# Performance work log

Hardware: AMD Instinct MI355X
Metric: run time of the kernel (lower is better)

## Reference

```python
import jax, jax.numpy as jnp
import numpy as np

B, S, D, H = 4, 2048, 1024, 16
DK = D // H
THETA = 10000.0


def apply_rope(x, pos, theta):
    # x: [B, H, S, DK], pos: [S] int
    d = x.shape[-1]
    inv_freq = theta ** (-jnp.arange(0, d, 2, dtype=jnp.float32) / d)  # [d/2]
    ang = pos.astype(jnp.float32)[:, None] * inv_freq[None, :]          # [S, d/2]
    cos, sin = jnp.cos(ang), jnp.sin(ang)
    x1 = x[..., 0::2]
    x2 = x[..., 1::2]
    r1 = x1 * cos - x2 * sin
    r2 = x1 * sin + x2 * cos
    return jnp.stack([r1, r2], axis=-1).reshape(x.shape)


def setup_inputs() -> dict:
    key = jax.random.key(0)
    ks = jax.random.split(key, 5)
    scale = 1.0 / np.sqrt(D)
    x = jax.random.normal(ks[0], (B, S, D), dtype=jnp.float32)
    Wq = jax.random.normal(ks[1], (D, D), dtype=jnp.float32) * scale
    Wk = jax.random.normal(ks[2], (D, D), dtype=jnp.float32) * scale
    Wv = jax.random.normal(ks[3], (D, D), dtype=jnp.float32) * scale
    Wo = jax.random.normal(ks[4], (D, D), dtype=jnp.float32) * scale
    token_positions = jnp.arange(S, dtype=jnp.int32)
    return {"x": x, "token_positions": token_positions,
            "Wq": Wq, "Wk": Wk, "Wv": Wv, "Wo": Wo}


def reference(x, token_positions, Wq, Wk, Wv, Wo):
    b, s, d = x.shape
    # Linear (no bias), weight stored [out, in]: y = x @ W.T
    q = (x @ Wq.T).reshape(b, s, H, DK).transpose(0, 2, 1, 3)  # [B,H,S,DK]
    k = (x @ Wk.T).reshape(b, s, H, DK).transpose(0, 2, 1, 3)
    v = (x @ Wv.T).reshape(b, s, H, DK).transpose(0, 2, 1, 3)
    q = apply_rope(q, token_positions, THETA)
    k = apply_rope(k, token_positions, THETA)
    scores = jnp.einsum('bhqd,bhkd->bhqk', q, k) / jnp.sqrt(jnp.float32(DK))
    causal = jnp.tril(jnp.ones((s, s), dtype=bool))
    scores = jnp.where(causal, scores, -jnp.inf)
    attn = jax.nn.softmax(scores, axis=-1)
    out = jnp.einsum('bhqk,bhkd->bhqd', attn, v)
    out = out.transpose(0, 2, 1, 3).reshape(b, s, d)
    return out @ Wo.T
```

## Files before the change

kernel.cpp:

```cpp
#include <hip/hip_runtime.h>

typedef unsigned short u16;
typedef __bf16 bf16x8 __attribute__((ext_vector_type(8)));
typedef float f32x4 __attribute__((ext_vector_type(4)));
typedef u16 u16x8 __attribute__((ext_vector_type(8)));
typedef u16 u16x4 __attribute__((ext_vector_type(4)));
typedef short s16x4 __attribute__((ext_vector_type(4)));

union V8 { u16x8 u; bf16x8 b; };
union V4 { u16x4 u; s16x4 s; unsigned w[2]; };

#define NB 4
#define NS 2048
#define ND 1024
#define NH 16
#define NDK 64
#define LP 80
#define CP 136
#define QSCL 0.18033688011112042f
#define FMAX 20.0f

__device__ __forceinline__ u16 f2bf(float f) {
  union { float f; unsigned u; } v; v.f = f;
  return (u16)((v.u + 0x7fffu + ((v.u >> 16) & 1u)) >> 16);
}

__device__ __forceinline__ unsigned pk2bf(float a, float b) {
#if __has_builtin(__builtin_amdgcn_cvt_pk_bf16_f32)
  auto v = __builtin_amdgcn_cvt_pk_bf16_f32(a, b);
  unsigned r; __builtin_memcpy(&r, &v, 4);
  return r;
#else
  return (unsigned)f2bf(a) | ((unsigned)f2bf(b) << 16);
#endif
}

__device__ __forceinline__ float fexp2(float x) {
#if __has_builtin(__builtin_amdgcn_exp2f)
  return __builtin_amdgcn_exp2f(x);
#else
  return exp2f(x);
#endif
}

__device__ __forceinline__ bf16x8 lds_frag(const u16* p) {
  V8 t; t.u = *(const u16x8*)p; return t.b;
}

__global__ __launch_bounds__(256) void cvt_bf16(const float* __restrict__ s,
                                                u16* __restrict__ d, int n) {
  const int i = (blockIdx.x * 256 + threadIdx.x) * 8;
  if (i >= n) return;
  const f32x4 lo = *(const f32x4*)(s + i);
  const f32x4 hi = *(const f32x4*)(s + i + 4);
  union { unsigned w[4]; u16x8 v; } o;
  o.w[0] = pk2bf(lo[0], lo[1]);
  o.w[1] = pk2bf(lo[2], lo[3]);
  o.w[2] = pk2bf(hi[0], hi[1]);
  o.w[3] = pk2bf(hi[2], hi[3]);
  *(u16x8*)(d + i) = o.v;
}

__global__ __launch_bounds__(256) void cvt_w4(const float* __restrict__ w0,
                                              const float* __restrict__ w1,
                                              const float* __restrict__ w2,
                                              const float* __restrict__ w3,
                                              u16* __restrict__ d) {
  const float* s = (blockIdx.y == 0) ? w0 : (blockIdx.y == 1) ? w1
                 : (blockIdx.y == 2) ? w2 : w3;
  const int i = (blockIdx.x * 256 + threadIdx.x) * 8;
  const f32x4 lo = *(const f32x4*)(s + i);
  const f32x4 hi = *(const f32x4*)(s + i + 4);
  union { unsigned w[4]; u16x8 v; } o;
  o.w[0] = pk2bf(lo[0], lo[1]);
  o.w[1] = pk2bf(lo[2], lo[3]);
  o.w[2] = pk2bf(hi[0], hi[1]);
  o.w[3] = pk2bf(hi[2], hi[3]);
  *(u16x8*)(d + (size_t)blockIdx.y * ND * ND + i) = o.v;
}

__global__ __launch_bounds__(256) void gemm_qkv(
    const u16* __restrict__ X, const u16* __restrict__ W0,
    const u16* __restrict__ W1, const u16* __restrict__ W2,
    void* __restrict__ O0, void* __restrict__ O1, void* __restrict__ O2,
    const int* __restrict__ tokpos, int modebase) {
  __shared__ u16 smem[2 * 128 * LP];
  u16* ldsA = smem;
  u16* ldsB = smem + 128 * LP;
  const int tid = threadIdx.x;
  const int lane = tid & 63;
  const int w = tid >> 6;
  const int quad = lane >> 4;
  const int l15 = lane & 15;
  const int z = blockIdx.z;
  const u16* Wp = (z == 0) ? W0 : (z == 1) ? W1 : W2;
  void* Op = (z == 0) ? O0 : (z == 1) ? O1 : O2;
  const int mode = modebase + z;
  const int m0 = blockIdx.x * 128;
  const int n0 = blockIdx.y * 128;
  const int wm = (w >> 1) * 64;
  const int wn = (w & 1) * 64;

  const int srow = tid >> 3;
  const int scol = (tid & 7) * 8;
  const u16* Ag = X + (size_t)(m0 + srow) * ND + scol;
  const u16* Bg = Wp + (size_t)(n0 + srow) * ND + scol;

  f32x4 acc[4][4];
  const f32x4 z4 = {0.f, 0.f, 0.f, 0.f};
  for (int i = 0; i < 4; i++)
    for (int j = 0; j < 4; j++) acc[i][j] = z4;

  for (int k0 = 0; k0 < ND; k0 += 64) {
    u16x8 ar[4], br[4];
    for (int r = 0; r < 4; r++) {
      ar[r] = *(const u16x8*)(Ag + (size_t)r * 32 * ND + k0);
      br[r] = *(const u16x8*)(Bg + (size_t)r * 32 * ND + k0);
    }
    __syncthreads();
    for (int r = 0; r < 4; r++) {
      *(u16x8*)&ldsA[(r * 32 + srow) * LP + scol] = ar[r];
      *(u16x8*)&ldsB[(r * 32 + srow) * LP + scol] = br[r];
    }
    __syncthreads();
    for (int kk = 0; kk < 2; kk++) {
      bf16x8 af[4], bfr[4];
      for (int mt = 0; mt < 4; mt++)
        af[mt] = lds_frag(&ldsA[(wm + mt * 16 + l15) * LP + (kk * 4 + quad) * 8]);
      for (int nt = 0; nt < 4; nt++)
        bfr[nt] = lds_frag(&ldsB[(wn + nt * 16 + l15) * LP + (kk * 4 + quad) * 8]);
      for (int mt = 0; mt < 4; mt++)
        for (int nt = 0; nt < 4; nt++)
          acc[mt][nt] = __builtin_amdgcn_mfma_f32_16x16x32_bf16(
              af[mt], bfr[nt], acc[mt][nt], 0, 0, 0);
    }
  }
  __syncthreads();

  if (mode < 2) {
    u16* cb = smem;
    for (int nt = 0; nt < 4; nt++) {
      const int n_g = n0 + wn + nt * 16 + l15;
      const int dk = n_g & 63;
      const float sgn = (dk & 1) ? 1.f : -1.f;
      const float inv_freq = __expf(-(float)(dk >> 1) * 0.28782313662425572f);
      for (int mt = 0; mt < 4; mt++) {
        const int mrow = wm + mt * 16 + quad * 4;
        for (int r = 0; r < 4; r++) {
          const int m_g = m0 + mrow + r;
          float v = acc[mt][nt][r];
          const int s_i = m_g & (NS - 1);
          const float pos = (float)tokpos[s_i];
          const float partner = __shfl_xor(v, 1);
          float sn, cs;
          __sincosf(pos * inv_freq, &sn, &cs);
          v = v * cs + partner * sn * sgn;
          if (mode == 0) v *= QSCL;
          cb[(mrow + r) * CP + wn + nt * 16 + l15] = f2bf(v);
        }
      }
    }
    __syncthreads();
    const int c = (tid & 15) * 8;
    const int h = (n0 + c) >> 6;
    const int dk0 = (n0 + c) & 63;
    for (int p = 0; p < 8; p++) {
      const int row = p * 16 + (tid >> 4);
      const int m_g = m0 + row;
      const int b = m_g >> 11;
      const int s_i = m_g & (NS - 1);
      *(u16x8*)&((u16*)Op)[(size_t)(((b * NH) + h) * NS + s_i) * NDK + dk0] =
          *(const u16x8*)&cb[row * CP + c];
    }
  } else if (mode == 2) {
    u16* cbT = smem;
    for (int nt = 0; nt < 4; nt++)
      for (int mt = 0; mt < 4; mt++)
        for (int r = 0; r < 4; r++)
          cbT[(wn + nt * 16 + l15) * CP + wm + mt * 16 + quad * 4 + r] =
              f2bf(acc[mt][nt][r]);
    __syncthreads();
    const int b = m0 >> 11;
    const int s0 = m0 & (NS - 1);
    const int col = (tid & 15) * 8;
    for (int p = 0; p < 8; p++) {
      const int row = p * 16 + (tid >> 4);
      const int dkg = n0 + row;
      const int h = dkg >> 6;
      *(u16x8*)&((u16*)Op)[(size_t)(((b * NH) + h) * NDK + (dkg & 63)) * NS +
                           s0 + col] = *(const u16x8*)&cbT[row * CP + col];
    }
  } else {
    for (int nt = 0; nt < 4; nt++) {
      const int n_g = n0 + wn + nt * 16 + l15;
      for (int mt = 0; mt < 4; mt++) {
        const int mb = m0 + wm + mt * 16 + quad * 4;
        for (int r = 0; r < 4; r++)
          ((float*)Op)[(size_t)(mb + r) * ND + n_g] = acc[mt][nt][r];
      }
    }
  }
}

__global__ __launch_bounds__(256) void attn(const u16* __restrict__ Q,
                                            const u16* __restrict__ Kc,
                                            const u16* __restrict__ Vt,
                                            u16* __restrict__ AO) {
  __shared__ u16 kt[64 * LP];
  __shared__ u16 vt[64 * LP];
  const int tid = threadIdx.x;
  const int lane = tid & 63;
  const int w = tid >> 6;
  const int quad = lane >> 4;
  const int l15 = lane & 15;
  const int bh = blockIdx.y;
  const int q0 = (gridDim.x - 1 - blockIdx.x) * 64;
  const int qg = q0 + w * 16 + l15;

  const u16* Qb = Q + (size_t)bh * NS * NDK + (size_t)qg * NDK + quad * 8;
  const bf16x8 qf0 = lds_frag(Qb);
  const bf16x8 qf1 = lds_frag(Qb + 32);

  f32x4 oacc[4];
  const f32x4 z4 = {0.f, 0.f, 0.f, 0.f};
  for (int i = 0; i < 4; i++) oacc[i] = z4;
  float lsum = 0.f;

  const int srow = tid >> 3;
  const int sg = tid & 7;
  const u16* Kb = Kc + (size_t)bh * NS * NDK;
  const u16* Vg = Vt + (size_t)bh * NDK * NS;

  u16x8 kreg[2], vreg[2];
  for (int r = 0; r < 2; r++) {
    kreg[r] = *(const u16x8*)(Kb + (size_t)(r * 32 + srow) * NDK + sg * 8);
    vreg[r] = *(const u16x8*)(Vg + (size_t)(r * 32 + srow) * NS + sg * 8);
  }

  for (int j0 = 0; j0 <= q0; j0 += 64) {
    __syncthreads();
    for (int r = 0; r < 2; r++) {
      const int row = r * 32 + srow;
      *(u16x8*)&kt[row * LP + (sg ^ (row & 7)) * 8] = kreg[r];
      *(u16x8*)&vt[row * LP + (sg ^ (row & 7)) * 8] = vreg[r];
    }
    __syncthreads();
    if (j0 + 64 <= q0) {
      const int nj = j0 + 64;
      for (int r = 0; r < 2; r++) {
        kreg[r] = *(const u16x8*)(Kb + (size_t)(nj + r * 32 + srow) * NDK + sg * 8);
        vreg[r] = *(const u16x8*)(Vg + (size_t)(r * 32 + srow) * NS + nj + sg * 8);
      }
    }

    f32x4 sa[4];
    for (int i = 0; i < 4; i++) sa[i] = z4;
    for (int kk = 0; kk < 2; kk++) {
      const bf16x8 qf = kk ? qf1 : qf0;
      for (int nt = 0; nt < 4; nt++) {
        const int row = nt * 16 + l15;
        const bf16x8 kf =
            lds_frag(&kt[row * LP + ((kk * 4 + quad) ^ (row & 7)) * 8]);
        sa[nt] = __builtin_amdgcn_mfma_f32_16x16x32_bf16(kf, qf, sa[nt], 0, 0, 0);
      }
    }

    const bool diag = (j0 == q0);
    float p[4][4];
    for (int nt = 0; nt < 4; nt++)
      for (int r = 0; r < 4; r++) {
        float e = fexp2(sa[nt][r] - FMAX);
        if (diag && (j0 + nt * 16 + quad * 4 + r) > qg) e = 0.f;
        p[nt][r] = e;
        lsum += e;
      }

    s16x4 pa[4];
    for (int nt = 0; nt < 4; nt++) {
      V4 t;
      t.w[0] = pk2bf(p[nt][0], p[nt][1]);
      t.w[1] = pk2bf(p[nt][2], p[nt][3]);
      pa[nt] = t.s;
    }

    for (int dt = 0; dt < 4; dt++) {
      const int dk = dt * 16 + l15;
      const int xr = dk & 7;
      for (int nt = 0; nt < 4; nt++) {
        const int chunk = 2 * nt + (quad >> 1);
        V4 t;
        t.u = *(const u16x4*)&vt[dk * LP + (chunk ^ xr) * 8 + 4 * (quad & 1)];
        oacc[dt] = __builtin_amdgcn_mfma_f32_16x16x16bf16_1k(pa[nt], t.s,
                                                             oacc[dt], 0, 0, 0);
      }
    }
  }

  lsum += __shfl_xor(lsum, 16);
  lsum += __shfl_xor(lsum, 32);
  float lq[4];
  for (int r = 0; r < 4; r++) lq[r] = __shfl(lsum, quad * 4 + r);

  __syncthreads();
  u16* ob = kt;
  for (int dt = 0; dt < 4; dt++)
    for (int r = 0; r < 4; r++)
      ob[(w * 16 + quad * 4 + r) * 72 + dt * 16 + l15] =
          f2bf(oacc[dt][r] / lq[r]);
  __syncthreads();
  const int b = bh >> 4, h = bh & 15;
  for (int p2 = 0; p2 < 2; p2++) {
    const int idx = p2 * 256 + tid;
    const int row = idx >> 3;
    const int c = (idx & 7) * 8;
    *(u16x8*)&AO[(size_t)(b * NS + q0 + row) * ND + h * 64 + c] =
        *(const u16x8*)&ob[row * 72 + c];
  }
}

extern "C" void kernel_launch(void* const* d_in, const int* in_sizes, int n_in,
                              void* d_out, int out_size, void* d_ws, size_t ws_size,
                              hipStream_t stream) {
  const float* x = (const float*)d_in[0];
  const int* tp = (const int*)d_in[1];
  const float* Wq = (const float*)d_in[2];
  const float* Wk = (const float*)d_in[3];
  const float* Wv = (const float*)d_in[4];
  const float* Wo = (const float*)d_in[5];

  const size_t NE = (size_t)NB * NS * ND;
  const int NW = ND * ND;
  u16* Qb = (u16*)d_ws;
  u16* Kb = Qb + NE;
  u16* Vtb = Kb + NE;
  u16* Xbf = Vtb + NE;
  u16* Wbf = Xbf + NE;

  dim3 blk(256);
  cvt_bf16<<<dim3((unsigned)(NE / 2048)), blk, 0, stream>>>(x, Xbf, (int)NE);
  cvt_w4<<<dim3(NW / 2048, 4), blk, 0, stream>>>(Wq, Wk, Wv, Wo, Wbf);
  gemm_qkv<<<dim3(64, 8, 3), blk, 0, stream>>>(
      Xbf, Wbf, Wbf + (size_t)NW, Wbf + 2 * (size_t)NW, Qb, Kb, Vtb, tp, 0);
  attn<<<dim3(NS / 64, NB * NH), blk, 0, stream>>>(Qb, Kb, Vtb, Xbf);
  gemm_qkv<<<dim3(64, 8, 1), blk, 0, stream>>>(
      Xbf, Wbf + 3 * (size_t)NW, Wbf + 3 * (size_t)NW, Wbf + 3 * (size_t)NW,
      d_out, d_out, d_out, tp, 3);
}
```

Baseline: 313.0 us.

## Use direct global-to-LDS loads in GEMM and atomic work queue in attention

The projection GEMM now loads A/B tiles with global_load_lds straight into an unpadded LDS layout, removing the register staging and store round-trip. The attention kernel fetches work items from an atomic counter and interleaves long and short causal tiles to balance load across CUs. The -FMAX softmax offset is folded into the MFMA accumulator init. The unpadded 64-wide LDS rows risk bank conflicts on fragment reads, and the counter relies on wrapping modulo the grid size across calls.

```diff
diff --git a/kernel.cpp b/kernel.cpp
--- a/kernel.cpp
+++ b/kernel.cpp
@@ -45,6 +45,12 @@
 
 __device__ __forceinline__ bf16x8 lds_frag(const u16* p) {
   V8 t; t.u = *(const u16x8*)p; return t.b;
+}
+
+__device__ __forceinline__ void gld16(const u16* g, u16* l) {
+  __builtin_amdgcn_global_load_lds(
+      (const __attribute__((address_space(1))) void*)g,
+      (__attribute__((address_space(3))) void*)l, 16, 0, 0);
 }
 
 __global__ __launch_bounds__(256) void cvt_bf16(const float* __restrict__ s,
@@ -84,9 +90,9 @@
     const u16* __restrict__ W1, const u16* __restrict__ W2,
     void* __restrict__ O0, void* __restrict__ O1, void* __restrict__ O2,
     const int* __restrict__ tokpos, int modebase) {
-  __shared__ u16 smem[2 * 128 * LP];
+  __shared__ u16 smem[128 * CP];
   u16* ldsA = smem;
-  u16* ldsB = smem + 128 * LP;
+  u16* ldsB = smem + 128 * 64;
   const int tid = threadIdx.x;
   const int lane = tid & 63;
   const int w = tid >> 6;
@@ -101,10 +107,12 @@
   const int wm = (w >> 1) * 64;
   const int wn = (w & 1) * 64;
 
-  const int srow = tid >> 3;
-  const int scol = (tid & 7) * 8;
-  const u16* Ag = X + (size_t)(m0 + srow) * ND + scol;
-  const u16* Bg = Wp + (size_t)(n0 + srow) * ND + scol;
+  const int lrow = lane >> 3;
+  const int lcol = (lane & 7) * 8;
+  const u16* Ag = X + (size_t)(m0 + w * 32 + lrow) * ND + lcol;
+  const u16* Bg = Wp + (size_t)(n0 + w * 32 + lrow) * ND + lcol;
+  u16* la = ldsA + (w * 32) * 64;
+  u16* lb = ldsB + (w * 32) * 64;
 
   f32x4 acc[4][4];
   const f32x4 z4 = {0.f, 0.f, 0.f, 0.f};
@@ -112,23 +120,18 @@
     for (int j = 0; j < 4; j++) acc[i][j] = z4;
 
   for (int k0 = 0; k0 < ND; k0 += 64) {
-    u16x8 ar[4], br[4];
-    for (int r = 0; r < 4; r++) {
-      ar[r] = *(const u16x8*)(Ag + (size_t)r * 32 * ND + k0);
-      br[r] = *(const u16x8*)(Bg + (size_t)r * 32 * ND + k0);
-    }
-    __syncthreads();
-    for (int r = 0; r < 4; r++) {
-      *(u16x8*)&ldsA[(r * 32 + srow) * LP + scol] = ar[r];
-      *(u16x8*)&ldsB[(r * 32 + srow) * LP + scol] = br[r];
+    __syncthreads();
+    for (int i = 0; i < 4; i++) {
+      gld16(Ag + (size_t)(i * 8) * ND + k0, la + i * 8 * 64);
+      gld16(Bg + (size_t)(i * 8) * ND + k0, lb + i * 8 * 64);
     }
     __syncthreads();
     for (int kk = 0; kk < 2; kk++) {
       bf16x8 af[4], bfr[4];
       for (int mt = 0; mt < 4; mt++)
-        af[mt] = lds_frag(&ldsA[(wm + mt * 16 + l15) * LP + (kk * 4 + quad) * 8]);
+        af[mt] = lds_frag(&ldsA[(wm + mt * 16 + l15) * 64 + (kk * 4 + quad) * 8]);
       for (int nt = 0; nt < 4; nt++)
-        bfr[nt] = lds_frag(&ldsB[(wn + nt * 16 + l15) * LP + (kk * 4 + quad) * 8]);
+        bfr[nt] = lds_frag(&ldsB[(wn + nt * 16 + l15) * 64 + (kk * 4 + quad) * 8]);
       for (int mt = 0; mt < 4; mt++)
         for (int nt = 0; nt < 4; nt++)
           acc[mt][nt] = __builtin_amdgcn_mfma_f32_16x16x32_bf16(
@@ -205,16 +208,24 @@
 __global__ __launch_bounds__(256) void attn(const u16* __restrict__ Q,
                                             const u16* __restrict__ Kc,
                                             const u16* __restrict__ Vt,
-                                            u16* __restrict__ AO) {
+                                            u16* __restrict__ AO,
+                                            unsigned* __restrict__ ctr) {
   __shared__ u16 kt[64 * LP];
   __shared__ u16 vt[64 * LP];
+  __shared__ unsigned s_item;
   const int tid = threadIdx.x;
   const int lane = tid & 63;
   const int w = tid >> 6;
   const int quad = lane >> 4;
   const int l15 = lane & 15;
-  const int bh = blockIdx.y;
-  const int q0 = (gridDim.x - 1 - blockIdx.x) * 64;
+
+  if (tid == 0) s_item = atomicAdd(ctr, 1u) & 2047u;
+  __syncthreads();
+  const unsigned item = s_item;
+  const int bh = (int)(item >> 5);
+  const int jj = (int)(item & 31u);
+  const int qt = (jj & 1) ? (jj >> 1) : (31 - (jj >> 1));
+  const int q0 = qt * 64;
   const int qg = q0 + w * 16 + l15;
 
   const u16* Qb = Q + (size_t)bh * NS * NDK + (size_t)qg * NDK + quad * 8;
@@ -237,6 +248,7 @@
     vreg[r] = *(const u16x8*)(Vg + (size_t)(r * 32 + srow) * NS + sg * 8);
   }
 
+  const f32x4 nF = {-FMAX, -FMAX, -FMAX, -FMAX};
   for (int j0 = 0; j0 <= q0; j0 += 64) {
     __syncthreads();
     for (int r = 0; r < 2; r++) {
@@ -254,7 +266,7 @@
     }
 
     f32x4 sa[4];
-    for (int i = 0; i < 4; i++) sa[i] = z4;
+    for (int i = 0; i < 4; i++) sa[i] = nF;
     for (int kk = 0; kk < 2; kk++) {
       const bf16x8 qf = kk ? qf1 : qf0;
       for (int nt = 0; nt < 4; nt++) {
@@ -269,7 +281,7 @@
     float p[4][4];
     for (int nt = 0; nt < 4; nt++)
       for (int r = 0; r < 4; r++) {
-        float e = fexp2(sa[nt][r] - FMAX);
+        float e = fexp2(sa[nt][r]);
         if (diag && (j0 + nt * 16 + quad * 4 + r) > qg) e = 0.f;
         p[nt][r] = e;
         lsum += e;
@@ -335,13 +347,14 @@
   u16* Vtb = Kb + NE;
   u16* Xbf = Vtb + NE;
   u16* Wbf = Xbf + NE;
+  unsigned* ctr = (unsigned*)(Wbf + 4 * (size_t)NW);
 
   dim3 blk(256);
   cvt_bf16<<<dim3((unsigned)(NE / 2048)), blk, 0, stream>>>(x, Xbf, (int)NE);
   cvt_w4<<<dim3(NW / 2048, 4), blk, 0, stream>>>(Wq, Wk, Wv, Wo, Wbf);
   gemm_qkv<<<dim3(64, 8, 3), blk, 0, stream>>>(
       Xbf, Wbf, Wbf + (size_t)NW, Wbf + 2 * (size_t)NW, Qb, Kb, Vtb, tp, 0);
-  attn<<<dim3(NS / 64, NB * NH), blk, 0, stream>>>(Qb, Kb, Vtb, Xbf);
+  attn<<<dim3(NS / 64, NB * NH), blk, 0, stream>>>(Qb, Kb, Vtb, Xbf, ctr);
   gemm_qkv<<<dim3(64, 8, 1), blk, 0, stream>>>(
       Xbf, Wbf + 3 * (size_t)NW, Wbf + 3 * (size_t)NW, Wbf + 3 * (size_t)NW,
       d_out, d_out, d_out, tp, 3);
```

Measured after the change: 310.0 us. No clear change (-1.0%).
